# Performance work log

Measured on AMD Instinct MI355X. Metric: run time of the kernel, lower is better.

Reference implementation:

```python
import jax, jax.numpy as jnp
import numpy as np

B_, C_, IMG, P, D, NL = 8, 3, 224, 16, 768, 12
DI, DS = 2 * D, 16          # d_inner (expand=2), d_state
DTR = (D + 15) // 16        # dt_rank = 48
N = (IMG // P) ** 2         # 196 patches
DCONV = 4


def setup_inputs() -> dict:
    key = jax.random.key(0)
    ks = jax.random.split(key, 10)
    s = lambda k, shape, scale: jax.random.normal(k, shape, jnp.float32) * scale
    return {
        "x": jax.random.normal(ks[0], (B_, C_, IMG, IMG), jnp.float32),
        "patch_w": s(ks[1], (D, C_, P, P), 0.02),
        "patch_b": jnp.zeros((D,), jnp.float32),
        "pos_embed": s(ks[2], (1, N, D), 0.02),
        "in_proj_w": s(ks[3], (NL, 2 * DI, D), 0.02),
        "conv_w": s(ks[4], (NL, DI, DCONV), 0.1),
        "conv_b": jnp.zeros((NL, DI), jnp.float32),
        "x_proj_w": s(ks[5], (NL, DTR + 2 * DS, DI), 0.02),
        "dt_proj_w": s(ks[6], (NL, DI, DTR), 0.1),
        # softplus-inverse of dt~0.01 (mamba default dt init)
        "dt_proj_b": jnp.log(jnp.expm1(jnp.full((NL, DI), 0.01, jnp.float32))),
        "A_log": jnp.log(jnp.broadcast_to(jnp.arange(1, DS + 1, dtype=jnp.float32), (NL, DI, DS))),
        "D_param": jnp.ones((NL, DI), jnp.float32),
        "out_proj_w": s(ks[7], (NL, D, DI), 0.02),
        "norm_w": jnp.ones((D,), jnp.float32),
        "norm_b": jnp.zeros((D,), jnp.float32),
    }


def _mamba_layer(x, inw, cw, cb, xpw, dtw, dtb, alog, dpar, ow):
    # x: (B, L, D)
    Bz, L, _ = x.shape
    xz = jnp.einsum('bld,ed->ble', x, inw)          # (B,L,2*DI)
    xc, z = jnp.split(xz, 2, axis=-1)
    # causal depthwise conv1d, kernel DCONV, left-pad DCONV-1
    xpad = jnp.pad(xc, ((0, 0), (DCONV - 1, 0), (0, 0)))
    xc = cb + sum(xpad[:, k:k + L, :] * cw[:, k] for k in range(DCONV))
    xc = jax.nn.silu(xc)
    proj = jnp.einsum('ble,fe->blf', xc, xpw)        # (B,L,DTR+2*DS)
    dt, Bm, Cm = proj[..., :DTR], proj[..., DTR:DTR + DS], proj[..., DTR + DS:]
    dt = jax.nn.softplus(jnp.einsum('blr,er->ble', dt, dtw) + dtb)  # (B,L,DI)
    A = -jnp.exp(alog)                               # (DI,DS)

    def step(h, inpt):
        xt, dtt, Bt, Ct = inpt                       # (B,DI),(B,DI),(B,DS),(B,DS)
        h = jnp.exp(dtt[:, :, None] * A) * h + (dtt * xt)[:, :, None] * Bt[:, None, :]
        return h, jnp.einsum('bds,bs->bd', h, Ct)

    h0 = jnp.zeros((Bz, DI, DS), x.dtype)
    _, ys = jax.lax.scan(step, h0, (xc.swapaxes(0, 1), dt.swapaxes(0, 1),
                                    Bm.swapaxes(0, 1), Cm.swapaxes(0, 1)))
    y = ys.swapaxes(0, 1) + xc * dpar                # D skip connection
    y = y * jax.nn.silu(z)                           # gate
    return jnp.einsum('ble,de->bld', y, ow)


def reference(x, patch_w, patch_b, pos_embed, in_proj_w, conv_w, conv_b,
              x_proj_w, dt_proj_w, dt_proj_b, A_log, D_param, out_proj_w,
              norm_w, norm_b):
    Bz = x.shape[0]
    Hn = IMG // P
    # stride==kernel conv -> non-overlapping patch einsum
    xp = x.reshape(Bz, C_, Hn, P, Hn, P)
    h = jnp.einsum('bcipjq,dcpq->bijd', xp, patch_w).reshape(Bz, N, D) + patch_b
    h = h + pos_embed
    for l in range(NL):  # no residual connections, per source
        h = _mamba_layer(h, in_proj_w[l], conv_w[l], conv_b[l], x_proj_w[l],
                         dt_proj_w[l], dt_proj_b[l], A_log[l], D_param[l], out_proj_w[l])
    mu = h.mean(-1, keepdims=True)
    var = ((h - mu) ** 2).mean(-1, keepdims=True)
    return (h - mu) * jax.lax.rsqrt(var + 1e-5) * norm_w + norm_b
```

## Files before the change

kernel.cpp:

```cpp
#include <hip/hip_runtime.h>

#define BB 8
#define IMG 224
#define DD 768
#define NLAY 12
#define DI 1536
#define DS 16
#define DTR 48
#define NPATCH 196
#define L_SEQ 196
#define M_ROWS 1568
#define MPAD 1664
#define DCONV 4
#define NC 14
#define LC 14
#define NCH 13

typedef _Float16 f16x8 __attribute__((ext_vector_type(8)));
typedef _Float16 f16x4 __attribute__((ext_vector_type(4)));
typedef float f32x4 __attribute__((ext_vector_type(4)));

__device__ __forceinline__ void gll16(const void* g, void* l) {
    __builtin_amdgcn_global_load_lds(
        (const __attribute__((address_space(1))) unsigned int*)g,
        (__attribute__((address_space(3))) unsigned int*)l,
        16, 0, 0);
}

__global__ __launch_bounds__(256) void split4_k(const float* __restrict__ in,
    _Float16* __restrict__ hi, _Float16* __restrict__ lo, int n4)
{
    int i = blockIdx.x * 256 + threadIdx.x;
    if (i >= n4) return;
    float4 v = ((const float4*)in)[i];
    _Float16 h0 = (_Float16)v.x, h1 = (_Float16)v.y, h2 = (_Float16)v.z, h3 = (_Float16)v.w;
    f16x4 H = {h0, h1, h2, h3};
    f16x4 L = {(_Float16)(v.x - (float)h0), (_Float16)(v.y - (float)h1),
               (_Float16)(v.z - (float)h2), (_Float16)(v.w - (float)h3)};
    ((f16x4*)hi)[i] = H;
    ((f16x4*)lo)[i] = L;
}

__global__ __launch_bounds__(256) void split4hi_k(const float* __restrict__ in,
    _Float16* __restrict__ hi, int n4)
{
    int i = blockIdx.x * 256 + threadIdx.x;
    if (i >= n4) return;
    float4 v = ((const float4*)in)[i];
    f16x4 H = {(_Float16)v.x, (_Float16)v.y, (_Float16)v.z, (_Float16)v.w};
    ((f16x4*)hi)[i] = H;
}

__global__ __launch_bounds__(256) void splitpadN_k(const float* __restrict__ in,
    _Float16* __restrict__ hi, _Float16* __restrict__ lo,
    int perIn, int inRows, int inCols, int outLd, int perOut, int total)
{
    int i = blockIdx.x * 256 + threadIdx.x;
    if (i >= total) return;
    int l = i / perOut, j = i % perOut;
    int r = j / outLd, c = j % outLd;
    float v = (r < inRows && c < inCols) ? in[(size_t)l * perIn + r * inCols + c] : 0.f;
    _Float16 h = (_Float16)v;
    hi[i] = h;
    lo[i] = (_Float16)(v - (float)h);
}

__global__ __launch_bounds__(256) void im2col_k(const float* __restrict__ x,
    _Float16* __restrict__ hi, _Float16* __restrict__ lo)
{
    int idx = blockIdx.x * 256 + threadIdx.x;
    if (idx >= M_ROWS * DD) return;
    int k = idx % DD;
    int m = idx / DD;
    int b = m / NPATCH;
    int t = m % NPATCH;
    int i = t / 14, j = t % 14;
    int c = k / 256;
    int pq = k % 256;
    int p = pq / 16, q = pq % 16;
    float v = x[(((size_t)b * 3 + c) * IMG + i * 16 + p) * IMG + j * 16 + q];
    _Float16 h = (_Float16)v;
    hi[idx] = h;
    lo[idx] = (_Float16)(v - (float)h);
}

__global__ __launch_bounds__(256) void mgemm128_k(
    const _Float16* __restrict__ Ah, const _Float16* __restrict__ Al,
    const _Float16* __restrict__ Bh,
    float* __restrict__ C, int M, int N, int K, int lda, long partStride)
{
    __shared__ __align__(16) _Float16 As[2][128][64];
    __shared__ __align__(16) _Float16 Bs[128][64];
    int tid = threadIdx.x, lane = tid & 63, wid = tid >> 6;
    int m0 = blockIdx.y * 128, n0 = blockIdx.x * 128;
    int kBeg = 0, nIter = K / 64;
    if (gridDim.z > 1) {
        int kPer = K / gridDim.z;
        kBeg = blockIdx.z * kPer;
        nIter = kPer / 64;
        C += (size_t)blockIdx.z * partStride;
    }

    int r0 = wid * 32;
    int lr = lane >> 3;
    int qs = ((lane & 7) ^ lr) * 8;
    const _Float16* AhP = Ah + (size_t)(m0 + r0 + lr) * lda + kBeg + qs;
    const _Float16* AlP = Al + (size_t)(m0 + r0 + lr) * lda + kBeg + qs;
    const _Float16* BhP = Bh + (size_t)(n0 + r0 + lr) * K + kBeg + qs;
    size_t a8 = (size_t)8 * lda, b8 = (size_t)8 * K;

    int wm = (wid >> 1) * 64, wn = (wid & 1) * 64;
    int lm = lane & 15, quad = lane >> 4;
    int seg0 = (quad ^ (lm & 7)) * 8;
    f32x4 acc[4][4] = {};

    for (int it = 0; it < nIter; ++it) {
        int k0 = it * 64;
#pragma unroll
        for (int j = 0; j < 4; ++j) {
            gll16(AhP + (size_t)j * a8 + k0, &As[0][r0 + 8 * j][0]);
            gll16(AlP + (size_t)j * a8 + k0, &As[1][r0 + 8 * j][0]);
            gll16(BhP + (size_t)j * b8 + k0, &Bs[r0 + 8 * j][0]);
        }
        __syncthreads();

#pragma unroll
        for (int ch = 0; ch < 2; ++ch) {
            int ls = seg0 ^ (ch * 32);
            f16x8 ah[4], al4[4], bh4[4];
#pragma unroll
            for (int i = 0; i < 4; ++i) {
                ah[i]  = *(const f16x8*)&As[0][wm + i * 16 + lm][ls];
                al4[i] = *(const f16x8*)&As[1][wm + i * 16 + lm][ls];
                bh4[i] = *(const f16x8*)&Bs[wn + i * 16 + lm][ls];
            }
#pragma unroll
            for (int mi = 0; mi < 4; ++mi)
#pragma unroll
                for (int ni = 0; ni < 4; ++ni) {
                    acc[mi][ni] = __builtin_amdgcn_mfma_f32_16x16x32_f16(ah[mi],  bh4[ni], acc[mi][ni], 0, 0, 0);
                    acc[mi][ni] = __builtin_amdgcn_mfma_f32_16x16x32_f16(al4[mi], bh4[ni], acc[mi][ni], 0, 0, 0);
                }
        }
        __syncthreads();
    }

#pragma unroll
    for (int mi = 0; mi < 4; ++mi)
#pragma unroll
        for (int ni = 0; ni < 4; ++ni)
#pragma unroll
            for (int r = 0; r < 4; ++r) {
                int row = m0 + wm + mi * 16 + quad * 4 + r;
                int col = n0 + wn + ni * 16 + lm;
                if (row < M) C[(size_t)row * N + col] = acc[mi][ni][r];
            }
}

__global__ __launch_bounds__(256) void mgemm_k(
    const _Float16* __restrict__ Ah, const _Float16* __restrict__ Al,
    const _Float16* __restrict__ Bh, const _Float16* __restrict__ Bl,
    float* __restrict__ C, _Float16* __restrict__ Chi, _Float16* __restrict__ Clo,
    int M, int N, int K, int lda, int Nstore,
    const float* __restrict__ bias, const float* __restrict__ pos, int mode)
{
    __shared__ __align__(16) _Float16 As[2][2][64][32];
    __shared__ __align__(16) _Float16 Bs[2][2][64][32];
    int tid = threadIdx.x, lane = tid & 63, wid = tid >> 6;
    int m0 = blockIdx.y * 64, n0 = blockIdx.x * 64;
    int kBeg = 0, nIter = K / 32;
    if (gridDim.z > 1) { int kPer = K / gridDim.z; kBeg = blockIdx.z * kPer; nIter = kPer / 32; }

    int srow = wid * 16 + (lane >> 2);
    int qs = ((lane & 3) ^ ((lane >> 3) & 3)) * 8;
    const _Float16* aH = Ah + (size_t)(m0 + srow) * lda + kBeg + qs;
    const _Float16* aL = Al + (size_t)(m0 + srow) * lda + kBeg + qs;
    const _Float16* bH = Bh + (size_t)(n0 + srow) * K + kBeg + qs;
    const _Float16* bL = Bl + (size_t)(n0 + srow) * K + kBeg + qs;

#define STAGE(buf, it) { int ko = (it) * 32;              \
        gll16(aH + ko, &As[buf][0][wid * 16][0]);          \
        gll16(aL + ko, &As[buf][1][wid * 16][0]);          \
        gll16(bH + ko, &Bs[buf][0][wid * 16][0]);          \
        gll16(bL + ko, &Bs[buf][1][wid * 16][0]); }

    int wm = (wid >> 1) * 32, wn = (wid & 1) * 32;
    int lm = lane & 15, quad = lane >> 4;
    int segA = (quad ^ ((lm >> 1) & 3)) * 8;
    f32x4 acc[2][2] = {};

    STAGE(0, 0);
    for (int it = 0; it < nIter; ++it) {
        int buf = it & 1;
        if (it + 1 < nIter) STAGE(buf ^ 1, it + 1);
        __syncthreads();
        f16x8 ah[2], al2[2], bh2[2], bl2[2];
#pragma unroll
        for (int i = 0; i < 2; ++i) {
            ah[i]  = *(const f16x8*)&As[buf][0][wm + i * 16 + lm][segA];
            al2[i] = *(const f16x8*)&As[buf][1][wm + i * 16 + lm][segA];
            bh2[i] = *(const f16x8*)&Bs[buf][0][wn + i * 16 + lm][segA];
            bl2[i] = *(const f16x8*)&Bs[buf][1][wn + i * 16 + lm][segA];
        }
#pragma unroll
        for (int mi = 0; mi < 2; ++mi)
#pragma unroll
            for (int ni = 0; ni < 2; ++ni) {
                acc[mi][ni] = __builtin_amdgcn_mfma_f32_16x16x32_f16(ah[mi],  bh2[ni], acc[mi][ni], 0, 0, 0);
                acc[mi][ni] = __builtin_amdgcn_mfma_f32_16x16x32_f16(ah[mi],  bl2[ni], acc[mi][ni], 0, 0, 0);
                acc[mi][ni] = __builtin_amdgcn_mfma_f32_16x16x32_f16(al2[mi], bh2[ni], acc[mi][ni], 0, 0, 0);
            }
        __syncthreads();
    }
#undef STAGE

#pragma unroll
    for (int mi = 0; mi < 2; ++mi)
#pragma unroll
        for (int ni = 0; ni < 2; ++ni)
#pragma unroll
            for (int r = 0; r < 4; ++r) {
                int row = m0 + wm + mi * 16 + quad * 4 + r;
                int col = n0 + wn + ni * 16 + lm;
                if (row >= M || col >= Nstore) continue;
                float v = acc[mi][ni][r];
                if (mode == 1) { v += bias[col]; v = (v > 20.f) ? v : log1pf(__expf(v)); }
                else if (mode == 2) v += bias[col] + pos[(size_t)(row % NPATCH) * N + col];
                size_t idx = (size_t)row * N + col;
                if (mode == 3) { atomicAdd(&C[idx], v); continue; }
                if (C) C[idx] = v;
                if (Chi) {
                    _Float16 h = (_Float16)v;
                    Chi[idx] = h;
                    Clo[idx] = (_Float16)(v - (float)h);
                }
            }
}

__global__ __launch_bounds__(256) void conv_k(
    const float* __restrict__ xz, const float* __restrict__ cw,
    const float* __restrict__ cb, _Float16* __restrict__ xch, _Float16* __restrict__ xcl,
    float* __restrict__ projb)
{
    int i4 = blockIdx.x * 256 + threadIdx.x;
    if (i4 >= M_ROWS * DI / 4) return;
    if (i4 < M_ROWS * 20) ((float4*)projb)[i4] = float4{0.f, 0.f, 0.f, 0.f};
    int e4 = i4 % (DI / 4);
    int m  = i4 / (DI / 4);
    int e  = e4 * 4;
    int l  = m % L_SEQ;
    float4 acc = *(const float4*)&cb[e];
    const float4* cwv = (const float4*)&cw[e * DCONV];
    float4 c0 = cwv[0], c1 = cwv[1], c2 = cwv[2], c3 = cwv[3];
#pragma unroll
    for (int k = 0; k < DCONV; ++k) {
        int ls = l + k - (DCONV - 1);
        if (ls >= 0) {
            float4 v = *(const float4*)&xz[(size_t)(m + k - (DCONV - 1)) * (2 * DI) + e];
            acc.x += (&c0.x)[k] * v.x;
            acc.y += (&c1.x)[k] * v.y;
            acc.z += (&c2.x)[k] * v.z;
            acc.w += (&c3.x)[k] * v.w;
        }
    }
    float r0 = acc.x / (1.f + __expf(-acc.x));
    float r1 = acc.y / (1.f + __expf(-acc.y));
    float r2 = acc.z / (1.f + __expf(-acc.z));
    float r3 = acc.w / (1.f + __expf(-acc.w));
    _Float16 h0 = (_Float16)r0, h1 = (_Float16)r1, h2 = (_Float16)r2, h3 = (_Float16)r3;
    f16x4 H = {h0, h1, h2, h3};
    f16x4 L = {(_Float16)(r0 - (float)h0), (_Float16)(r1 - (float)h1),
               (_Float16)(r2 - (float)h2), (_Float16)(r3 - (float)h3)};
    ((f16x4*)xch)[i4] = H;
    ((f16x4*)xcl)[i4] = L;
}

__global__ __launch_bounds__(64) void scanA_k(
    const _Float16* __restrict__ xch, const _Float16* __restrict__ xcl,
    const float* __restrict__ proj, const float* __restrict__ dtw,
    const float* __restrict__ dtb, const float* __restrict__ A_log,
    float* __restrict__ hpart, float* __restrict__ Sdt)
{
    int d = blockIdx.x * 64 + threadIdx.x;
    int b = blockIdx.y, c = blockIdx.z;
    float Aa[DS];
#pragma unroll
    for (int s = 0; s < DS; ++s) Aa[s] = -__expf(A_log[d * DS + s]);
    float W[DTR];
    const float4* Wp = (const float4*)(dtw + (size_t)d * DTR);
#pragma unroll
    for (int i = 0; i < DTR / 4; ++i) {
        float4 w = Wp[i];
        W[4 * i] = w.x; W[4 * i + 1] = w.y; W[4 * i + 2] = w.z; W[4 * i + 3] = w.w;
    }
    float bia = dtb[d];
    float h[DS];
#pragma unroll
    for (int s = 0; s < DS; ++s) h[s] = 0.f;
    float sdt = 0.f;
    size_t base = (size_t)b * L_SEQ + c * LC;
    for (int l = 0; l < LC; ++l) {
        size_t ii = (base + l) * DI + d;
        const float* pr = proj + (base + l) * 80;
        float draw = bia;
#pragma unroll
        for (int r = 0; r < DTR; ++r) draw += pr[r] * W[r];
        float dtv = (draw > 20.f) ? draw : log1pf(__expf(draw));
        float xv  = (float)xch[ii] + (float)xcl[ii];
        float dx = dtv * xv;
        sdt += dtv;
#pragma unroll
        for (int s = 0; s < DS; ++s)
            h[s] = __expf(dtv * Aa[s]) * h[s] + dx * pr[DTR + s];
    }
    size_t o = (size_t)(b * NCH + c) * DS * DI + d;
#pragma unroll
    for (int s = 0; s < DS; ++s) hpart[o + (size_t)s * DI] = h[s];
    Sdt[(size_t)(b * NCH + c) * DI + d] = sdt;
}

__global__ __launch_bounds__(64) void scanC_k(
    const _Float16* __restrict__ xch, const _Float16* __restrict__ xcl,
    const float* __restrict__ proj, const float* __restrict__ xz,
    const float* __restrict__ dtw, const float* __restrict__ dtb,
    const float* __restrict__ A_log, const float* __restrict__ Dp,
    const float* __restrict__ hpart, const float* __restrict__ Sdt,
    _Float16* __restrict__ yh, _Float16* __restrict__ yl)
{
    int d = blockIdx.x * 64 + threadIdx.x;
    int b = blockIdx.y, c = blockIdx.z;
    float Aa[DS];
#pragma unroll
    for (int s = 0; s < DS; ++s) Aa[s] = -__expf(A_log[d * DS + s]);
    float W[DTR];
    const float4* Wp = (const float4*)(dtw + (size_t)d * DTR);
#pragma unroll
    for (int i = 0; i < DTR / 4; ++i) {
        float4 w = Wp[i];
        W[4 * i] = w.x; W[4 * i + 1] = w.y; W[4 * i + 2] = w.z; W[4 * i + 3] = w.w;
    }
    float bia = dtb[d];
    float h[DS];
#pragma unroll
    for (int s = 0; s < DS; ++s) h[s] = 0.f;
    for (int cc = 0; cc < c; ++cc) {
        float sdt = Sdt[(size_t)(b * NCH + cc) * DI + d];
        size_t o = (size_t)(b * NCH + cc) * DS * DI + d;
#pragma unroll
        for (int s = 0; s < DS; ++s)
            h[s] = __expf(Aa[s] * sdt) * h[s] + hpart[o + (size_t)s * DI];
    }
    float dP = Dp[d];
    size_t base = (size_t)b * L_SEQ + c * LC;
    for (int l = 0; l < LC; ++l) {
        size_t ii = (base + l) * DI + d;
        const float* pr = proj + (base + l) * 80;
        float draw = bia;
#pragma unroll
        for (int r = 0; r < DTR; ++r) draw += pr[r] * W[r];
        float dtv = (draw > 20.f) ? draw : log1pf(__expf(draw));
        float xv  = (float)xch[ii] + (float)xcl[ii];
        float zv  = xz[(base + l) * 2 * DI + DI + d];
        float dx = dtv * xv;
        float accv = 0.f;
#pragma unroll
        for (int s = 0; s < DS; ++s) {
            h[s] = __expf(dtv * Aa[s]) * h[s] + dx * pr[DTR + s];
            accv += h[s] * pr[DTR + DS + s];
        }
        float yv = accv + xv * dP;
        float sg = 1.f / (1.f + __expf(-zv));
        float vy = yv * (zv * sg);
        _Float16 hh = (_Float16)vy;
        yh[ii] = hh;
        yl[ii] = (_Float16)(vy - (float)hh);
    }
}

__global__ __launch_bounds__(256) void red4split_k(const float* __restrict__ part,
    _Float16* __restrict__ hi, _Float16* __restrict__ lo, int n4, int stride4)
{
    int i = blockIdx.x * 256 + threadIdx.x;
    if (i >= n4) return;
    const float4* p = (const float4*)part;
    float4 a = p[i], b = p[i + stride4], c = p[i + 2 * stride4], e = p[i + 3 * stride4];
    float x0 = a.x + b.x + c.x + e.x;
    float x1 = a.y + b.y + c.y + e.y;
    float x2 = a.z + b.z + c.z + e.z;
    float x3 = a.w + b.w + c.w + e.w;
    _Float16 h0 = (_Float16)x0, h1 = (_Float16)x1, h2 = (_Float16)x2, h3 = (_Float16)x3;
    f16x4 H = {h0, h1, h2, h3};
    f16x4 L = {(_Float16)(x0 - (float)h0), (_Float16)(x1 - (float)h1),
               (_Float16)(x2 - (float)h2), (_Float16)(x3 - (float)h3)};
    ((f16x4*)hi)[i] = H;
    ((f16x4*)lo)[i] = L;
}

__global__ __launch_bounds__(256) void ln_k(const _Float16* __restrict__ hh,
    const _Float16* __restrict__ hl,
    const float* __restrict__ w, const float* __restrict__ bias, float* __restrict__ out)
{
    int row = blockIdx.x;
    int tid = threadIdx.x;
    size_t base = (size_t)row * DD;
    float v0 = (float)hh[base + tid]       + (float)hl[base + tid];
    float v1 = (float)hh[base + tid + 256] + (float)hl[base + tid + 256];
    float v2 = (float)hh[base + tid + 512] + (float)hl[base + tid + 512];
    float s = v0 + v1 + v2;
    __shared__ float red[4];
    for (int off = 32; off; off >>= 1) s += __shfl_down(s, off);
    if ((tid & 63) == 0) red[tid >> 6] = s;
    __syncthreads();
    float mu = (red[0] + red[1] + red[2] + red[3]) * (1.f / 768.f);
    __syncthreads();
    float d0 = v0 - mu, d1 = v1 - mu, d2 = v2 - mu;
    float vs = d0 * d0 + d1 * d1 + d2 * d2;
    for (int off = 32; off; off >>= 1) vs += __shfl_down(vs, off);
    if ((tid & 63) == 0) red[tid >> 6] = vs;
    __syncthreads();
    float var = (red[0] + red[1] + red[2] + red[3]) * (1.f / 768.f);
    float rs = rsqrtf(var + 1e-5f);
    out[base + tid]       = d0 * rs * w[tid]       + bias[tid];
    out[base + tid + 256] = d1 * rs * w[tid + 256] + bias[tid + 256];
    out[base + tid + 512] = d2 * rs * w[tid + 512] + bias[tid + 512];
}

extern "C" void kernel_launch(void* const* d_in, const int* in_sizes, int n_in,
                              void* d_out, int out_size, void* d_ws, size_t ws_size,
                              hipStream_t stream) {
    const float* x        = (const float*)d_in[0];
    const float* patch_w  = (const float*)d_in[1];
    const float* patch_b  = (const float*)d_in[2];
    const float* pos      = (const float*)d_in[3];
    const float* in_proj  = (const float*)d_in[4];
    const float* conv_w   = (const float*)d_in[5];
    const float* conv_b   = (const float*)d_in[6];
    const float* x_proj   = (const float*)d_in[7];
    const float* dt_w     = (const float*)d_in[8];
    const float* dt_b     = (const float*)d_in[9];
    const float* A_log    = (const float*)d_in[10];
    const float* D_param  = (const float*)d_in[11];
    const float* out_w    = (const float*)d_in[12];
    const float* norm_w   = (const float*)d_in[13];
    const float* norm_b   = (const float*)d_in[14];
    float* out = (float*)d_out;

    float* ws    = (float*)d_ws;
    float* xzb   = ws;
    float* projb = xzb   + 4816896;
    float* hpart = projb + 125440;
    float* sdtb  = hpart + 2555904;
    float* opart = sdtb  + 159744;
    _Float16* fp  = (_Float16*)(opart + 4816896);
    _Float16* hbh = fp;
    _Float16* hbl = hbh + MPAD * DD;
    _Float16* yh  = hbl + MPAD * DD;
    _Float16* yl  = yh  + MPAD * DI;
    _Float16* xch = yl  + MPAD * DI;
    _Float16* xcl = xch + MPAD * DI;
    _Float16* pwh = xcl + MPAD * DI;
    _Float16* pwl = pwh + 589824;
    _Float16* wih = pwl + 589824;
    _Float16* woh = wih + (size_t)NLAY * 2359296;
    _Float16* xwh = woh + (size_t)NLAY * 1179648;
    _Float16* xwl = xwh + (size_t)NLAY * 196608;

    split4hi_k<<<(NLAY * 2359296 / 4 + 255) / 256, 256, 0, stream>>>(in_proj, wih, NLAY * 2359296 / 4);
    split4hi_k<<<(NLAY * 1179648 / 4 + 255) / 256, 256, 0, stream>>>(out_w, woh, NLAY * 1179648 / 4);
    splitpadN_k<<<(NLAY * 196608 + 255) / 256, 256, 0, stream>>>(
        x_proj, xwh, xwl, 80 * DI, 80, DI, DI, 196608, NLAY * 196608);
    split4_k<<<(589824 / 4 + 255) / 256, 256, 0, stream>>>(patch_w, pwh, pwl, 589824 / 4);

    im2col_k<<<(M_ROWS * DD + 255) / 256, 256, 0, stream>>>(x, yh, yl);
    mgemm_k<<<dim3(12, 25), 256, 0, stream>>>(yh, yl, pwh, pwl,
        nullptr, hbh, hbl, M_ROWS, DD, DD, DD, DD, patch_b, pos, 2);

    for (int l = 0; l < NLAY; ++l) {
        const float* Al  = A_log + (size_t)l * DI * DS;
        const float* Wdt = dt_w  + (size_t)l * DI * DTR;
        const float* Bdt = dt_b  + (size_t)l * DI;
        mgemm128_k<<<dim3(24, 13), 256, 0, stream>>>(hbh, hbl,
            wih + (size_t)l * 2359296,
            xzb, M_ROWS, 2 * DI, DD, DD, 0);
        conv_k<<<(M_ROWS * DI / 4) / 256, 256, 0, stream>>>(xzb, conv_w + (size_t)l * DI * DCONV,
                                                            conv_b + (size_t)l * DI, xch, xcl, projb);
        mgemm_k<<<dim3(2, 25, 4), 256, 0, stream>>>(xch, xcl,
            xwh + (size_t)l * 196608, xwl + (size_t)l * 196608,
            projb, nullptr, nullptr, M_ROWS, 80, DI, DI, 80, nullptr, nullptr, 3);
        scanA_k<<<dim3(DI / 64, BB, NCH), 64, 0, stream>>>(xch, xcl, projb, Wdt, Bdt, Al, hpart, sdtb);
        scanC_k<<<dim3(DI / 64, BB, NC), 64, 0, stream>>>(xch, xcl, projb, xzb, Wdt, Bdt, Al,
                                                          D_param + (size_t)l * DI, hpart, sdtb, yh, yl);
        mgemm128_k<<<dim3(6, 13, 4), 256, 0, stream>>>(yh, yl,
            woh + (size_t)l * 1179648,
            opart, M_ROWS, DD, DI, DI, (long)M_ROWS * DD);
        red4split_k<<<(M_ROWS * DD / 4 + 255) / 256, 256, 0, stream>>>(
            opart, hbh, hbl, M_ROWS * DD / 4, M_ROWS * DD / 4);
    }

    ln_k<<<M_ROWS, 256, 0, stream>>>(hbh, hbl, norm_w, norm_b, out);
}
```

Measured before the change: 1.920 ms.

## Double-buffer LDS in mgemm128 and use partial vmcnt waits before barriers

Adds a second LDS buffer to the 128x128 split-fp16 GEMM so the next K tile is prefetched via global_load_lds while the current one is computed. In both GEMM kernels, __syncthreads is replaced with explicit s_waitcnt vmcnt(N) plus s_barrier, so only the older loads are waited on and the prefetch stays in flight. This doubles LDS use in mgemm128 (to 96KB), which may lower occupancy. It also relies on hand-counted vmcnt values being correct.

Result: slower. 2.146 ms (+11.8%).

```diff
diff --git a/kernel.cpp b/kernel.cpp
--- a/kernel.cpp
+++ b/kernel.cpp
@@ -89,8 +89,8 @@
     const _Float16* __restrict__ Bh,
     float* __restrict__ C, int M, int N, int K, int lda, long partStride)
 {
-    __shared__ __align__(16) _Float16 As[2][128][64];
-    __shared__ __align__(16) _Float16 Bs[128][64];
+    __shared__ __align__(16) _Float16 As[2][2][128][64];
+    __shared__ __align__(16) _Float16 Bs[2][128][64];
     int tid = threadIdx.x, lane = tid & 63, wid = tid >> 6;
     int m0 = blockIdx.y * 128, n0 = blockIdx.x * 128;
     int kBeg = 0, nIter = K / 64;
@@ -109,20 +109,27 @@
     const _Float16* BhP = Bh + (size_t)(n0 + r0 + lr) * K + kBeg + qs;
     size_t a8 = (size_t)8 * lda, b8 = (size_t)8 * K;
 
+#define STAGE128(sb, it) { int k0 = (it) * 64;                          \
+        _Pragma("unroll") for (int j = 0; j < 4; ++j) {                 \
+            gll16(AhP + (size_t)j * a8 + k0, &As[sb][0][r0 + 8 * j][0]); \
+            gll16(AlP + (size_t)j * a8 + k0, &As[sb][1][r0 + 8 * j][0]); \
+            gll16(BhP + (size_t)j * b8 + k0, &Bs[sb][r0 + 8 * j][0]); } }
+
     int wm = (wid >> 1) * 64, wn = (wid & 1) * 64;
     int lm = lane & 15, quad = lane >> 4;
     int seg0 = (quad ^ (lm & 7)) * 8;
     f32x4 acc[4][4] = {};
 
+    STAGE128(0, 0);
     for (int it = 0; it < nIter; ++it) {
-        int k0 = it * 64;
-#pragma unroll
-        for (int j = 0; j < 4; ++j) {
-            gll16(AhP + (size_t)j * a8 + k0, &As[0][r0 + 8 * j][0]);
-            gll16(AlP + (size_t)j * a8 + k0, &As[1][r0 + 8 * j][0]);
-            gll16(BhP + (size_t)j * b8 + k0, &Bs[r0 + 8 * j][0]);
+        int buf = it & 1;
+        if (it + 1 < nIter) {
+            STAGE128(buf ^ 1, it + 1);
+            asm volatile("s_waitcnt vmcnt(12)" ::: "memory");
+        } else {
+            asm volatile("s_waitcnt vmcnt(0)" ::: "memory");
         }
-        __syncthreads();
+        __builtin_amdgcn_s_barrier();
 
 #pragma unroll
         for (int ch = 0; ch < 2; ++ch) {
@@ -130,9 +137,9 @@
             f16x8 ah[4], al4[4], bh4[4];
 #pragma unroll
             for (int i = 0; i < 4; ++i) {
-                ah[i]  = *(const f16x8*)&As[0][wm + i * 16 + lm][ls];
-                al4[i] = *(const f16x8*)&As[1][wm + i * 16 + lm][ls];
-                bh4[i] = *(const f16x8*)&Bs[wn + i * 16 + lm][ls];
+                ah[i]  = *(const f16x8*)&As[buf][0][wm + i * 16 + lm][ls];
+                al4[i] = *(const f16x8*)&As[buf][1][wm + i * 16 + lm][ls];
+                bh4[i] = *(const f16x8*)&Bs[buf][wn + i * 16 + lm][ls];
             }
 #pragma unroll
             for (int mi = 0; mi < 4; ++mi)
@@ -142,8 +149,10 @@
                     acc[mi][ni] = __builtin_amdgcn_mfma_f32_16x16x32_f16(al4[mi], bh4[ni], acc[mi][ni], 0, 0, 0);
                 }
         }
-        __syncthreads();
-    }
+        asm volatile("s_waitcnt lgkmcnt(0)" ::: "memory");
+        __builtin_amdgcn_s_barrier();
+    }
+#undef STAGE128
 
 #pragma unroll
     for (int mi = 0; mi < 4; ++mi)
@@ -192,8 +201,13 @@
     STAGE(0, 0);
     for (int it = 0; it < nIter; ++it) {
         int buf = it & 1;
-        if (it + 1 < nIter) STAGE(buf ^ 1, it + 1);
-        __syncthreads();
+        if (it + 1 < nIter) {
+            STAGE(buf ^ 1, it + 1);
+            asm volatile("s_waitcnt vmcnt(4)" ::: "memory");
+        } else {
+            asm volatile("s_waitcnt vmcnt(0)" ::: "memory");
+        }
+        __builtin_amdgcn_s_barrier();
         f16x8 ah[2], al2[2], bh2[2], bl2[2];
 #pragma unroll
         for (int i = 0; i < 2; ++i) {
@@ -210,7 +224,8 @@
                 acc[mi][ni] = __builtin_amdgcn_mfma_f32_16x16x32_f16(ah[mi],  bl2[ni], acc[mi][ni], 0, 0, 0);
                 acc[mi][ni] = __builtin_amdgcn_mfma_f32_16x16x32_f16(al2[mi], bh2[ni], acc[mi][ni], 0, 0, 0);
             }
-        __syncthreads();
+        asm volatile("s_waitcnt lgkmcnt(0)" ::: "memory");
+        __builtin_amdgcn_s_barrier();
     }
 #undef STAGE
 
```
